# Performance work log

Hardware: AMD Instinct MI355X
Metric: run time of the kernel (lower is better)

Reference implementation:

```python
import jax, jax.numpy as jnp
import numpy as np

S, B, O, L, NL = 256, 64, 128, 256, 25
SIGMA_X, SIGMA_Z, ALPHA = 0.1, 0.1, 0.9


def setup_inputs() -> dict:
    key = jax.random.key(0)
    ks = jax.random.split(key, 12)
    def w(k, shape, s=0.05):
        return jax.random.normal(k, shape, dtype=jnp.float32) * s
    return {
        "obsrv": jax.random.normal(ks[0], (S, B, O), dtype=jnp.float32),
        "z0": jax.random.normal(ks[1], (NL, B, L), dtype=jnp.float32),
        "W_emb_z": w(ks[2], (L, L)), "b_emb_z": jnp.zeros((L,), jnp.float32),
        "Wx1": w(ks[3], (L, O)), "bx1": jnp.zeros((L,), jnp.float32),
        "Wx2": w(ks[4], (L, L)), "bx2": jnp.zeros((L,), jnp.float32),
        "Wx3": w(ks[5], (L, L)), "bx3": jnp.zeros((L,), jnp.float32),
        "W_ih": w(ks[6], (NL, 4 * L, L)), "W_hh": w(ks[7], (NL, 4 * L, L)),
        "b_ih": jnp.zeros((NL, 4 * L), jnp.float32),
        "b_hh": jnp.zeros((NL, 4 * L), jnp.float32),
        "W_out": w(ks[8], (L, L)), "b_out": jnp.zeros((L,), jnp.float32),
    }


def reference(obsrv, z0, W_emb_z, b_emb_z, Wx1, bx1, Wx2, bx2, Wx3, bx3,
              W_ih, W_hh, b_ih, b_hh, W_out, b_out):
    # Eval-mode LIDM forward: dropout disabled; noise injection kept (fixed PRNG).
    noise_key = jax.random.key(42)
    sqrt_alpha = jnp.sqrt(jnp.float32(ALPHA))

    def step(carry, inp):
        h, c = carry            # each [NL, B, L]
        x_k, k_idx = inp        # [B, O], scalar step index
        kh, kx = jax.random.split(jax.random.fold_in(noise_key, k_idx))
        # hidden = embedding_z(hidden) + sigma_z * noise
        h = jnp.einsum('nbl,ml->nbm', h, W_emb_z) + b_emb_z
        h = h + SIGMA_Z * jax.random.normal(kh, h.shape, dtype=h.dtype)
        # f_phi_x 3-layer MLP
        e = jax.nn.relu(x_k @ Wx1.T + bx1)
        e = jax.nn.relu(e @ Wx2.T + bx2)
        e = e @ Wx3.T + bx3
        e = sqrt_alpha * e + SIGMA_X * jax.random.normal(kx, e.shape, dtype=e.dtype)
        # 25-layer stacked LSTM, single time step (torch gate order i,f,g,o)
        inp_l = e
        hs, cs = [], []
        for l in range(NL):
            gates = inp_l @ W_ih[l].T + b_ih[l] + h[l] @ W_hh[l].T + b_hh[l]
            i, f, g, o = jnp.split(gates, 4, axis=-1)
            c_new = jax.nn.sigmoid(f) * c[l] + jax.nn.sigmoid(i) * jnp.tanh(g)
            h_new = jax.nn.sigmoid(o) * jnp.tanh(c_new)
            hs.append(h_new)
            cs.append(c_new)
            inp_l = h_new
        out = inp_l @ W_out.T + b_out
        return (jnp.stack(hs), jnp.stack(cs)), out

    c0 = jnp.zeros_like(z0)
    ks = jnp.arange(1, S)
    (_, _), ys = jax.lax.scan(step, (z0, c0), (obsrv[1:], ks))
    # outputs[0] stays zero, as in the torch module
    outputs = jnp.concatenate([jnp.zeros((1, B, L), ys.dtype), ys], axis=0)
    return outputs
```

## Files before the change

kernel.cpp:

```cpp
#include <hip/hip_runtime.h>
#include <stdint.h>

#define S_ 256
#define B_ 64
#define O_ 128
#define L_ 256
#define NL_ 25

typedef __attribute__((ext_vector_type(8))) short short8v;
typedef __attribute__((ext_vector_type(16))) float f32x16;
typedef __attribute__((ext_vector_type(4))) uint32_t u32x4;
typedef __attribute__((ext_vector_type(2))) uint32_t u32x2;

#define EMLP_B  0u
#define HL_B    8388608u
#define Z0P_B   16777216u
#define RING_B  17596416u
#define VBUF_B  24150016u
#define WF_B    37257216u
#define WN_B    50364416u
#define BIASF_B 63471616u
#define FLAG_B  63574016u
#define NFLAG_B 63580416u
#define WS_END  63626016u

#define GLDF(BV, BASE)                                                           \
  do {                                                                           \
    uint64_t a0_ = (uint64_t)(uintptr_t)(BASE);                                  \
    uint64_t a1_ = a0_ + 4096,  a2_ = a0_ + 8192,  a3_ = a0_ + 12288;            \
    uint64_t a4_ = a0_ + 16384, a5_ = a0_ + 20480, a6_ = a0_ + 24576;            \
    uint64_t a7_ = a0_ + 28672;                                                  \
    asm volatile("global_load_dwordx4 %0, %1, off sc0 sc1"             : "=v"(BV[0])  : "v"(a0_)); \
    asm volatile("global_load_dwordx4 %0, %1, off offset:2048 sc0 sc1" : "=v"(BV[1])  : "v"(a0_)); \
    asm volatile("global_load_dwordx4 %0, %1, off sc0 sc1"             : "=v"(BV[2])  : "v"(a1_)); \
    asm volatile("global_load_dwordx4 %0, %1, off offset:2048 sc0 sc1" : "=v"(BV[3])  : "v"(a1_)); \
    asm volatile("global_load_dwordx4 %0, %1, off sc0 sc1"             : "=v"(BV[4])  : "v"(a2_)); \
    asm volatile("global_load_dwordx4 %0, %1, off offset:2048 sc0 sc1" : "=v"(BV[5])  : "v"(a2_)); \
    asm volatile("global_load_dwordx4 %0, %1, off sc0 sc1"             : "=v"(BV[6])  : "v"(a3_)); \
    asm volatile("global_load_dwordx4 %0, %1, off offset:2048 sc0 sc1" : "=v"(BV[7])  : "v"(a3_)); \
    asm volatile("global_load_dwordx4 %0, %1, off sc0 sc1"             : "=v"(BV[8])  : "v"(a4_)); \
    asm volatile("global_load_dwordx4 %0, %1, off offset:2048 sc0 sc1" : "=v"(BV[9])  : "v"(a4_)); \
    asm volatile("global_load_dwordx4 %0, %1, off sc0 sc1"             : "=v"(BV[10]) : "v"(a5_)); \
    asm volatile("global_load_dwordx4 %0, %1, off offset:2048 sc0 sc1" : "=v"(BV[11]) : "v"(a5_)); \
    asm volatile("global_load_dwordx4 %0, %1, off sc0 sc1"             : "=v"(BV[12]) : "v"(a6_)); \
    asm volatile("global_load_dwordx4 %0, %1, off offset:2048 sc0 sc1" : "=v"(BV[13]) : "v"(a6_)); \
    asm volatile("global_load_dwordx4 %0, %1, off sc0 sc1"             : "=v"(BV[14]) : "v"(a7_)); \
    asm volatile("global_load_dwordx4 %0, %1, off offset:2048 sc0 sc1" : "=v"(BV[15]) : "v"(a7_)); \
  } while (0)

#define VMWAIT                                                                   \
  do {                                                                           \
    asm volatile("s_waitcnt vmcnt(0)" ::: "memory");                             \
    __builtin_amdgcn_sched_barrier(0);                                           \
  } while (0)

#define GST16(PTR, VAL)                                                          \
  do {                                                                           \
    uint64_t a_ = (uint64_t)(uintptr_t)(PTR);                                    \
    asm volatile("global_store_dwordx4 %0, %1, off sc0 sc1" :: "v"(a_), "v"(VAL) : "memory"); \
  } while (0)

#define GST8(PTR, VAL)                                                           \
  do {                                                                           \
    uint64_t a_ = (uint64_t)(uintptr_t)(PTR);                                    \
    asm volatile("global_store_dwordx2 %0, %1, off sc0 sc1" :: "v"(a_), "v"(VAL) : "memory"); \
  } while (0)

#define VMDRAIN asm volatile("s_waitcnt vmcnt(0)" ::: "memory")

__device__ __forceinline__ uint16_t f2bf(float x) {
  uint32_t u = __float_as_uint(x);
  return (uint16_t)((u + 0x7fffu + ((u >> 16) & 1u)) >> 16);
}
__device__ __forceinline__ float bf2f(uint16_t u) {
  return __uint_as_float(((uint32_t)u) << 16);
}
__device__ __forceinline__ short8v pack8(float4 a, float4 b) {
  short8v w;
  w[0] = (short)f2bf(a.x); w[1] = (short)f2bf(a.y);
  w[2] = (short)f2bf(a.z); w[3] = (short)f2bf(a.w);
  w[4] = (short)f2bf(b.x); w[5] = (short)f2bf(b.y);
  w[6] = (short)f2bf(b.z); w[7] = (short)f2bf(b.w);
  return w;
}

__device__ __forceinline__ uint32_t rotl32(uint32_t v, int r) {
  return (v << r) | (v >> (32 - r));
}

__device__ __forceinline__ void tf2x32(uint32_t k0, uint32_t k1,
                                       uint32_t x0, uint32_t x1,
                                       uint32_t& o0, uint32_t& o1) {
  uint32_t ks2 = k0 ^ k1 ^ 0x1BD11BDAu;
  x0 += k0; x1 += k1;
  x0 += x1; x1 = rotl32(x1, 13); x1 ^= x0;
  x0 += x1; x1 = rotl32(x1, 15); x1 ^= x0;
  x0 += x1; x1 = rotl32(x1, 26); x1 ^= x0;
  x0 += x1; x1 = rotl32(x1,  6); x1 ^= x0;
  x0 += k1; x1 += ks2 + 1u;
  x0 += x1; x1 = rotl32(x1, 17); x1 ^= x0;
  x0 += x1; x1 = rotl32(x1, 29); x1 ^= x0;
  x0 += x1; x1 = rotl32(x1, 16); x1 ^= x0;
  x0 += x1; x1 = rotl32(x1, 24); x1 ^= x0;
  x0 += ks2; x1 += k0 + 2u;
  x0 += x1; x1 = rotl32(x1, 13); x1 ^= x0;
  x0 += x1; x1 = rotl32(x1, 15); x1 ^= x0;
  x0 += x1; x1 = rotl32(x1, 26); x1 ^= x0;
  x0 += x1; x1 = rotl32(x1,  6); x1 ^= x0;
  x0 += k0; x1 += k1 + 3u;
  x0 += x1; x1 = rotl32(x1, 17); x1 ^= x0;
  x0 += x1; x1 = rotl32(x1, 29); x1 ^= x0;
  x0 += x1; x1 = rotl32(x1, 16); x1 ^= x0;
  x0 += x1; x1 = rotl32(x1, 24); x1 ^= x0;
  x0 += k1; x1 += ks2 + 4u;
  x0 += x1; x1 = rotl32(x1, 13); x1 ^= x0;
  x0 += x1; x1 = rotl32(x1, 15); x1 ^= x0;
  x0 += x1; x1 = rotl32(x1, 26); x1 ^= x0;
  x0 += x1; x1 = rotl32(x1,  6); x1 ^= x0;
  o0 = x0 + ks2; o1 = x1 + k0 + 5u;
}

__device__ __forceinline__ void step_keys(int k, uint32_t& kh0, uint32_t& kh1,
                                          uint32_t& kx0, uint32_t& kx1) {
  uint32_t f0, f1;
  tf2x32(0u, 42u, 0u, (uint32_t)k, f0, f1);
  tf2x32(f0, f1, 0u, 0u, kh0, kh1);
  tf2x32(f0, f1, 0u, 1u, kx0, kx1);
}

__device__ __forceinline__ uint32_t rbits(uint32_t key0, uint32_t key1,
                                          uint32_t i) {
  uint32_t b0, b1;
  tf2x32(key0, key1, 0u, i, b0, b1);
  return b0 ^ b1;
}

__device__ __forceinline__ float u32_to_normal(uint32_t bits) {
  const float lo = __uint_as_float(0xBF7FFFFFu);
  float f = __uint_as_float((bits >> 9) | 0x3F800000u) - 1.0f;
  float u = f * 2.0f + lo;
  u = fmaxf(lo, u);
  float x = u;
  float w = -log1pf(-x * x);
  float p;
  if (w < 5.0f) {
    w -= 2.5f;
    p =            2.81022636e-08f;
    p = fmaf(p, w, 3.43273939e-07f);
    p = fmaf(p, w, -3.5233877e-06f);
    p = fmaf(p, w, -4.39150654e-06f);
    p = fmaf(p, w, 0.00021858087f);
    p = fmaf(p, w, -0.00125372503f);
    p = fmaf(p, w, -0.00417768164f);
    p = fmaf(p, w, 0.246640727f);
    p = fmaf(p, w, 1.50140941f);
  } else {
    w = sqrtf(w) - 3.0f;
    p =            -0.000200214257f;
    p = fmaf(p, w, 0.000100950558f);
    p = fmaf(p, w, 0.00134934322f);
    p = fmaf(p, w, -0.00367342844f);
    p = fmaf(p, w, 0.00573950773f);
    p = fmaf(p, w, -0.0076224613f);
    p = fmaf(p, w, 0.00943887047f);
    p = fmaf(p, w, 1.00167406f);
    p = fmaf(p, w, 2.83297682f);
  }
  return __uint_as_float(0x3FB504F3u) * (p * x);
}

__device__ __forceinline__ float sigm(float x) { return 1.0f / (1.0f + expf(-x)); }

__device__ __forceinline__ uint64_t ld_u64_sc(const uint64_t* p) {
  uint64_t v;
  asm volatile("global_load_dwordx2 %0, %1, off sc0 sc1\n\ts_waitcnt vmcnt(0)"
               : "=v"(v) : "v"((uint64_t)(uintptr_t)p) : "memory");
  return v;
}
__device__ __forceinline__ uint32_t ld_u16_sc(const uint16_t* p) {
  uint32_t v;
  asm volatile("global_load_ushort %0, %1, off sc0 sc1\n\ts_waitcnt vmcnt(0)"
               : "=v"(v) : "v"((uint64_t)(uintptr_t)p) : "memory");
  return v;
}
__device__ __forceinline__ void spin_bytes_ge(const uint64_t* p, uint32_t want) {
  for (;;) {
    uint64_t v = ld_u64_sc(p);
    bool ok = true;
#pragma unroll
    for (int i = 0; i < 8; ++i) ok &= (uint32_t)((v >> (8 * i)) & 0xffu) >= want;
    if (ok) return;
    __builtin_amdgcn_s_sleep(4);
  }
}
__device__ __forceinline__ void spin_nf(const uint16_t* p, uint32_t pid) {
  uint32_t want = (pid & 0xffu) | ((pid & 0xffu) << 8);
  while (ld_u16_sc(p) != want) __builtin_amdgcn_s_sleep(4);
}
__device__ __forceinline__ void st_u8_sc(uint8_t* p, uint32_t v) {
  asm volatile("global_store_byte %0, %1, off sc0 sc1"
               :: "v"((uint64_t)(uintptr_t)p), "v"(v) : "memory");
}

__device__ __forceinline__ void gen_quarter(uint16_t* __restrict__ vbl,
                                            int l, int p, int s, int t, int q) {
  uint32_t kh0, kh1, kx0, kx1;
  step_keys(p, kh0, kh1, kx0, kx1);
  int vb = 32 * (s & 1) + (t >> 4);
  int fs = (t & 15) * 16 + q * 4;
  uint32_t ib = ((uint32_t)(l * 64 + vb)) * 256 + (uint32_t)fs;
  int g = fs >> 3;
  uint16_t* dst = vbl + (((size_t)(p & 15)) << 14) + ((size_t)(g * 64 + vb)) * 8 + (fs & 7);
  uint16_t n0 = f2bf(0.1f * u32_to_normal(rbits(kh0, kh1, ib + 0)));
  uint16_t n1 = f2bf(0.1f * u32_to_normal(rbits(kh0, kh1, ib + 1)));
  uint16_t n2 = f2bf(0.1f * u32_to_normal(rbits(kh0, kh1, ib + 2)));
  uint16_t n3 = f2bf(0.1f * u32_to_normal(rbits(kh0, kh1, ib + 3)));
  u32x2 dv;
  dv[0] = (uint32_t)n0 | ((uint32_t)n1 << 16);
  dv[1] = (uint32_t)n2 | ((uint32_t)n3 << 16);
  GST8(dst, dv);
}

__global__ __launch_bounds__(256) void k_init(const float* __restrict__ z0,
                                              uint16_t* __restrict__ z0p,
                                              uint32_t* __restrict__ fl) {
  int idx = blockIdx.x * 256 + threadIdx.x;
  int fi = idx & 255;
  int b = (idx >> 8) & 63;
  int l = idx >> 14;
  z0p[(((size_t)l * 32 + (fi >> 3)) * 64 + b) * 8 + (fi & 7)] = f2bf(z0[idx]);
  if (idx < 8000) fl[idx] = 0u;
}

__global__ __launch_bounds__(256) void k_wf(const float* __restrict__ Whh,
                                            const float* __restrict__ Wemb,
                                            uint16_t* __restrict__ Wf) {
  __shared__ float Bs[32][256];
  int l = blockIdx.x >> 4, rt = blockIdx.x & 15;
  int j = threadIdx.x;
  float acc[64];
#pragma unroll
  for (int r = 0; r < 64; ++r) acc[r] = 0.0f;
  const float* Abase = Whh + ((size_t)l * 1024 + rt * 64) * 256;
  for (int m0 = 0; m0 < 256; m0 += 32) {
    __syncthreads();
    {
      int rr = threadIdx.x >> 3, cseg = threadIdx.x & 7;
      const float* src = Wemb + (size_t)(m0 + rr) * 256 + cseg * 32;
      float* dst = &Bs[rr][cseg * 32];
#pragma unroll
      for (int q = 0; q < 8; ++q)
        reinterpret_cast<float4*>(dst)[q] = reinterpret_cast<const float4*>(src)[q];
    }
    __syncthreads();
    for (int mm = 0; mm < 32; ++mm) {
      float bj = Bs[mm][j];
      const float* Acol = Abase + m0 + mm;
#pragma unroll
      for (int r = 0; r < 64; ++r) acc[r] = fmaf(Acol[r * 256], bj, acc[r]);
    }
  }
  for (int r = 0; r < 64; ++r)
    Wf[((size_t)l * 1024 + rt * 64 + r) * 256 + j] = f2bf(acc[r]);
}

__global__ __launch_bounds__(256) void k_wn(const float* __restrict__ Whh,
                                            uint16_t* __restrict__ Wn) {
  int l = blockIdx.x >> 3, s = blockIdx.x & 7;
  uint16_t* base = Wn + ((size_t)(l * 8 + s) << 15);
  for (int it = 0; it < 16; ++it) {
    int c = it * 256 + threadIdx.x;
    int c2 = c >> 7;
    int r = c & 127;
    int gi = (r & 3) * 256 + s * 32 + (r >> 5) * 8 + ((r >> 2) & 7);
    const float* src = Whh + ((size_t)l * 1024 + gi) * 256 + c2 * 8;
    float4 f0 = *reinterpret_cast<const float4*>(src);
    float4 f1 = *reinterpret_cast<const float4*>(src + 4);
    *reinterpret_cast<short8v*>(base + (size_t)c * 8) = pack8(f0, f1);
  }
}

__global__ __launch_bounds__(256) void k_biasf(const float* __restrict__ Whh,
                                               const float* __restrict__ bemb,
                                               const float* __restrict__ bih,
                                               const float* __restrict__ bhh,
                                               float* __restrict__ biasf) {
  int l = blockIdx.x >> 2;
  int gi = (blockIdx.x & 3) * 256 + threadIdx.x;
  const float* row = Whh + ((size_t)l * 1024 + gi) * 256;
  float a = 0.0f;
  for (int m = 0; m < 256; ++m) a = fmaf(row[m], bemb[m], a);
  biasf[l * 1024 + gi] = a + bih[l * 1024 + gi] + bhh[l * 1024 + gi];
}

__global__ __launch_bounds__(256) void k_mlp1(const float* __restrict__ obsrv,
                                              const float* __restrict__ Wx1,
                                              const float* __restrict__ bx1,
                                              uint16_t* __restrict__ e1out) {
  int k = 1 + (blockIdx.x >> 2);
  int jc = blockIdx.x & 3;
  int lane = threadIdx.x & 63;
  int wv = threadIdx.x >> 6;
  int j0 = jc * 64 + wv * 16;
  const float* xrow = obsrv + ((size_t)k * B_ + lane) * O_;
  float acc[16];
#pragma unroll
  for (int i = 0; i < 16; ++i) acc[i] = 0.0f;
  for (int o = 0; o < O_; o += 4) {
    float4 a = *reinterpret_cast<const float4*>(&xrow[o]);
#pragma unroll
    for (int mi = 0; mi < 16; ++mi) {
      float4 wt = *reinterpret_cast<const float4*>(&Wx1[(size_t)(j0 + mi) * O_ + o]);
      float t = acc[mi];
      t = fmaf(a.x, wt.x, t); t = fmaf(a.y, wt.y, t);
      t = fmaf(a.z, wt.z, t); t = fmaf(a.w, wt.w, t);
      acc[mi] = t;
    }
  }
  uint16_t* dst = e1out + (size_t)k * L_ * B_;
#pragma unroll
  for (int mi = 0; mi < 16; ++mi) {
    float v = acc[mi] + bx1[j0 + mi];
    dst[(j0 + mi) * B_ + lane] = f2bf(fmaxf(v, 0.0f));
  }
}

__global__ __launch_bounds__(256) void k_mlp2(const uint16_t* __restrict__ e1buf,
                                              const float* __restrict__ Wx2,
                                              const float* __restrict__ bx2,
                                              const float* __restrict__ Wx3,
                                              const float* __restrict__ bx3,
                                              uint16_t* __restrict__ E_mlp) {
  __shared__ float e2s[L_ * B_];
  int k = 1 + blockIdx.x;
  int lane = threadIdx.x & 63;
  int wv = threadIdx.x >> 6;
  const uint16_t* e1 = e1buf + (size_t)k * L_ * B_;

  for (int rep = 0; rep < 4; ++rep) {
    int m0 = rep * 64 + wv * 16;
    float acc[16];
#pragma unroll
    for (int i = 0; i < 16; ++i) acc[i] = 0.0f;
    for (int j = 0; j < L_; j += 4) {
      float a0 = bf2f(e1[(j + 0) * B_ + lane]);
      float a1 = bf2f(e1[(j + 1) * B_ + lane]);
      float a2 = bf2f(e1[(j + 2) * B_ + lane]);
      float a3 = bf2f(e1[(j + 3) * B_ + lane]);
#pragma unroll
      for (int mi = 0; mi < 16; ++mi) {
        float4 wt = *reinterpret_cast<const float4*>(&Wx2[(size_t)(m0 + mi) * L_ + j]);
        float t = acc[mi];
        t = fmaf(a0, wt.x, t); t = fmaf(a1, wt.y, t);
        t = fmaf(a2, wt.z, t); t = fmaf(a3, wt.w, t);
        acc[mi] = t;
      }
    }
#pragma unroll
    for (int mi = 0; mi < 16; ++mi) {
      float v = acc[mi] + bx2[m0 + mi];
      e2s[(m0 + mi) * B_ + lane] = fmaxf(v, 0.0f);
    }
  }
  __syncthreads();

  uint32_t kh0, kh1, kx0, kx1;
  step_keys(k, kh0, kh1, kx0, kx1);
  const float sa = sqrtf(0.9f);

  for (int rep = 0; rep < 4; ++rep) {
    int m0 = rep * 64 + wv * 16;
    float acc[16];
#pragma unroll
    for (int i = 0; i < 16; ++i) acc[i] = 0.0f;
    for (int j = 0; j < L_; j += 4) {
      float a0 = e2s[(j + 0) * B_ + lane];
      float a1 = e2s[(j + 1) * B_ + lane];
      float a2 = e2s[(j + 2) * B_ + lane];
      float a3 = e2s[(j + 3) * B_ + lane];
#pragma unroll
      for (int mi = 0; mi < 16; ++mi) {
        float4 wt = *reinterpret_cast<const float4*>(&Wx3[(size_t)(m0 + mi) * L_ + j]);
        float t = acc[mi];
        t = fmaf(a0, wt.x, t); t = fmaf(a1, wt.y, t);
        t = fmaf(a2, wt.z, t); t = fmaf(a3, wt.w, t);
        acc[mi] = t;
      }
    }
    uint16_t tmp[16];
#pragma unroll
    for (int mi = 0; mi < 16; ++mi) {
      int m = m0 + mi;
      float nz = u32_to_normal(rbits(kx0, kx1, (uint32_t)(lane * L_ + m)));
      tmp[mi] = f2bf(sa * (acc[mi] + bx3[m]) + 0.1f * nz);
    }
    int g0 = m0 >> 3;
    uint16_t* d0 = E_mlp + (((size_t)k * 32 + g0) * 64 + lane) * 8;
    uint16_t* d1 = E_mlp + (((size_t)k * 32 + g0 + 1) * 64 + lane) * 8;
    *reinterpret_cast<uint4*>(d0) = *reinterpret_cast<const uint4*>(&tmp[0]);
    *reinterpret_cast<uint4*>(d1) = *reinterpret_cast<const uint4*>(&tmp[8]);
  }
}

__global__ __launch_bounds__(512, 1) void k_wave(
    const uint16_t* __restrict__ Wf, const float* __restrict__ W_ih,
    const uint16_t* __restrict__ Wn, const float* __restrict__ biasf,
    const uint16_t* __restrict__ z0p, const uint16_t* __restrict__ emlp,
    uint16_t* __restrict__ ring, uint16_t* __restrict__ vbuf,
    uint16_t* __restrict__ hlast, uint8_t* __restrict__ flagb,
    uint8_t* __restrict__ nfb) {
  __shared__ __align__(16) unsigned char WAF[65536];
  __shared__ __align__(16) unsigned char WAI[65536];

  const int slot = (blockIdx.x & 7) * 25 + (blockIdx.x >> 3);
  const int l = slot >> 3;
  const int s = slot & 7;
  const int t = threadIdx.x;
  const int lane = t & 63;
  const int wid = t >> 6;
  const int lo5 = lane & 31;
  const int hi = lane >> 5;
  const int tm = wid >> 1;
  const int tn = wid & 1;
  const int bcol = tn * 32 + lo5;
  const int arow = tm * 32 + lo5;
  const int aswz = (arow & 7) << 4;

#pragma unroll 1
  for (int it = 0; it < 8; ++it) {
    int c = it * 512 + t;
    int r = c >> 5, cc = c & 31;
    int gi = (r & 3) * 256 + s * 32 + (r >> 5) * 8 + ((r >> 2) & 7);
    uint4 v = *reinterpret_cast<const uint4*>(Wf + ((size_t)l * 1024 + gi) * 256 + cc * 8);
    *reinterpret_cast<uint4*>(WAF + r * 512 + ((cc * 16) ^ ((r & 7) << 4))) = v;
  }
#pragma unroll 1
  for (int it = 0; it < 8; ++it) {
    int c = it * 512 + t;
    int r = c >> 5, cc = c & 31;
    int gi = (r & 3) * 256 + s * 32 + (r >> 5) * 8 + ((r >> 2) & 7);
    const float* sr = W_ih + ((size_t)l * 1024 + gi) * 256 + cc * 8;
    float4 f0 = *reinterpret_cast<const float4*>(sr);
    float4 f1 = *reinterpret_cast<const float4*>(sr + 4);
    *reinterpret_cast<short8v*>(WAI + r * 512 + ((cc * 16) ^ ((r & 7) << 4))) = pack8(f0, f1);
  }

  float bfr[16];
#pragma unroll
  for (int mq = 0; mq < 4; ++mq) {
    int mi = s * 32 + tm * 8 + mq * 2 + hi;
#pragma unroll
    for (int g = 0; g < 4; ++g)
      bfr[mq * 4 + g] = biasf[l * 1024 + g * 256 + mi];
  }
  __syncthreads();

  uint16_t* vbl = vbuf + ((size_t)(l * 16) << 14);
  const uint16_t* wb = Wn + ((size_t)(l * 8 + s) << 15);
  const int blane = hi * 1024 + bcol * 16;
  const int ggrp = s * 4 + tm;

#define NFE(P) ((uint16_t*)(nfb + ((size_t)(l * 16 + ((P) & 15))) * 64))

#pragma unroll 1
  for (int g = 0; g < 2; ++g) {
    int p = 1 + g * 4 + (s >> 1);
#pragma unroll 1
    for (int q = 0; q < 4; ++q) gen_quarter(vbl, l, p, s, t, q);
    VMDRAIN;
    __syncthreads();
    if (t == 0) st_u8_sc((uint8_t*)NFE(p) + (s & 1), (uint32_t)(p & 0xff));
  }

  f32x16 nbt[4];
  float cst[4] = {0.0f, 0.0f, 0.0f, 0.0f};

#define PRO_NBT(ST, IDX)                                                         \
  do {                                                                           \
    if (t == 0) spin_nf(NFE(ST), (uint32_t)(ST));                                \
    __syncthreads();                                                             \
    const unsigned char* V = (const unsigned char*)vbl +                         \
        (((size_t)((ST) & 15)) << 15) + blane;                                   \
    short8v bv[16];                                                              \
    GLDF(bv, V);                                                                 \
    VMWAIT;                                                                      \
    f32x16 nw = {0,0,0,0,0,0,0,0,0,0,0,0,0,0,0,0};                               \
    _Pragma("unroll")                                                            \
    for (int kt = 0; kt < 16; ++kt) {                                            \
      short8v av = *reinterpret_cast<const short8v*>(                            \
          wb + ((size_t)((kt * 2 + hi) * 128 + arow)) * 8);                      \
      nw = __builtin_amdgcn_mfma_f32_32x32x16_bf16(av, bv[kt], nw, 0, 0, 0);     \
    }                                                                            \
    nbt[IDX] = nw;                                                               \
  } while (0)

  PRO_NBT(1, 0);
  PRO_NBT(2, 1);
  PRO_NBT(3, 2);
  PRO_NBT(4, 3);

#pragma unroll 1
  for (int k = 1; k <= 255; ++k) {
    if (t == 0 && k > 1) spin_bytes_ge((const uint64_t*)(flagb + l * 256), (uint32_t)(k - 1));
    if (t == 64 && l < NL_ - 1 && k >= 9)
      spin_bytes_ge((const uint64_t*)(flagb + (l + 1) * 256), (uint32_t)(k - 8));
    __syncthreads();

    const unsigned char* hp = (k == 1)
        ? ((const unsigned char*)z0p + (((size_t)l) << 15) + blane)
        : ((const unsigned char*)ring + (((size_t)(l * 8 + ((k - 1) & 7))) << 15) + blane);
    short8v bv0[16];
    GLDF(bv0, hp);

    if (t == 0 && l > 0) spin_bytes_ge((const uint64_t*)(flagb + (l - 1) * 256), (uint32_t)k);
    __syncthreads();
    VMWAIT;

    const unsigned char* ip = (l == 0)
        ? ((const unsigned char*)emlp + (((size_t)k) << 15) + blane)
        : ((const unsigned char*)ring + (((size_t)((l - 1) * 8 + (k & 7))) << 15) + blane);
    short8v bv1[16];
    GLDF(bv1, ip);

    f32x16 acc = nbt[0];
#pragma unroll
    for (int kt = 0; kt < 16; ++kt) {
      short8v av = *reinterpret_cast<const short8v*>(WAF + arow * 512 + ((kt * 32 + hi * 16) ^ aswz));
      acc = __builtin_amdgcn_mfma_f32_32x32x16_bf16(av, bv0[kt], acc, 0, 0, 0);
    }
    VMWAIT;
#pragma unroll
    for (int kt = 0; kt < 16; ++kt) {
      short8v av = *reinterpret_cast<const short8v*>(WAI + arow * 512 + ((kt * 32 + hi * 16) ^ aswz));
      acc = __builtin_amdgcn_mfma_f32_32x32x16_bf16(av, bv1[kt], acc, 0, 0, 0);
    }

    uint16_t hv[4];
#pragma unroll
    for (int mq = 0; mq < 4; ++mq) {
      float iv = acc[4 * mq + 0] + bfr[mq * 4 + 0];
      float fv = acc[4 * mq + 1] + bfr[mq * 4 + 1];
      float gv = acc[4 * mq + 2] + bfr[mq * 4 + 2];
      float ov = acc[4 * mq + 3] + bfr[mq * 4 + 3];
      float cn = sigm(fv) * cst[mq] + sigm(iv) * tanhf(gv);
      float hn = sigm(ov) * tanhf(cn);
      cst[mq] = cn;
      hv[mq] = f2bf(hn);
      if (l == NL_ - 1) {
        int mi = s * 32 + tm * 8 + mq * 2 + hi;
        hlast[((size_t)k << 14) + mi * 64 + bcol] = hv[mq];
      }
    }
    {
      uint32_t w0 = (uint32_t)hv[0] | ((uint32_t)hv[1] << 16);
      uint32_t w1 = (uint32_t)hv[2] | ((uint32_t)hv[3] << 16);
      uint32_t p0 = (uint32_t)__shfl_xor((int)w0, 32);
      uint32_t p1 = (uint32_t)__shfl_xor((int)w1, 32);
      if (hi == 0) {
        u32x4 dv;
        dv[0] = (w0 & 0xffffu) | (p0 << 16);
        dv[1] = (w0 >> 16) | (p0 & 0xffff0000u);
        dv[2] = (w1 & 0xffffu) | (p1 << 16);
        dv[3] = (w1 >> 16) | (p1 & 0xffff0000u);
        unsigned char* rp = (unsigned char*)ring +
            (((size_t)(l * 8 + (k & 7))) << 15) + ((size_t)(ggrp * 64 + bcol)) * 16;
        GST16(rp, dv);
      }
    }
    VMDRAIN;
    __syncthreads();
    if (t == 0) st_u8_sc(flagb + l * 256 + s, (uint32_t)(k & 0xff));

    {
      int base = ((k - 1) & ~3) + 1;
      int q = (k - 1) & 3;
      int p = base + 8 + (s >> 1);
      if (p <= 255) {
        gen_quarter(vbl, l, p, s, t, q);
        if (q == 3) {
          VMDRAIN;
          __syncthreads();
          if (t == 0) st_u8_sc((uint8_t*)NFE(p) + (s & 1), (uint32_t)(p & 0xff));
        }
      }
    }
    {
      int kn = k + 4;
      f32x16 nw = {0,0,0,0,0,0,0,0,0,0,0,0,0,0,0,0};
      if (kn <= 255) {
        if (t == 0) spin_nf(NFE(kn), (uint32_t)kn);
        __syncthreads();
        const unsigned char* V = (const unsigned char*)vbl +
            (((size_t)(kn & 15)) << 15) + blane;
        short8v bv[16];
        GLDF(bv, V);
        VMWAIT;
#pragma unroll
        for (int kt = 0; kt < 16; ++kt) {
          short8v av = *reinterpret_cast<const short8v*>(
              wb + ((size_t)((kt * 2 + hi) * 128 + arow)) * 8);
          nw = __builtin_amdgcn_mfma_f32_32x32x16_bf16(av, bv[kt], nw, 0, 0, 0);
        }
      }
      nbt[0] = nbt[1]; nbt[1] = nbt[2]; nbt[2] = nbt[3]; nbt[3] = nw;
    }
  }
#undef NFE
#undef PRO_NBT
}

__global__ __launch_bounds__(256) void k_final(const uint16_t* __restrict__ Hlast,
                                               const float* __restrict__ W_out,
                                               const float* __restrict__ b_out,
                                               float* __restrict__ out) {
  int k = blockIdx.x >> 2;
  int mc = blockIdx.x & 3;
  int lane = threadIdx.x & 63;
  int wv = threadIdx.x >> 6;
  int m0 = mc * 64 + wv * 16;
  float res[16];
  if (k == 0) {
#pragma unroll
    for (int mi = 0; mi < 16; ++mi) res[mi] = 0.0f;
  } else {
    float acc[16];
#pragma unroll
    for (int i = 0; i < 16; ++i) acc[i] = 0.0f;
    const uint16_t* src = Hlast + ((size_t)k << 14);
    for (int j = 0; j < L_; j += 4) {
      float a0 = bf2f(src[(j + 0) * B_ + lane]);
      float a1 = bf2f(src[(j + 1) * B_ + lane]);
      float a2 = bf2f(src[(j + 2) * B_ + lane]);
      float a3 = bf2f(src[(j + 3) * B_ + lane]);
#pragma unroll
      for (int mi = 0; mi < 16; ++mi) {
        float4 wt = *reinterpret_cast<const float4*>(&W_out[(size_t)(m0 + mi) * L_ + j]);
        float t = acc[mi];
        t = fmaf(a0, wt.x, t); t = fmaf(a1, wt.y, t);
        t = fmaf(a2, wt.z, t); t = fmaf(a3, wt.w, t);
        acc[mi] = t;
      }
    }
#pragma unroll
    for (int mi = 0; mi < 16; ++mi) res[mi] = acc[mi] + b_out[m0 + mi];
  }
  float* dst = out + ((size_t)k * B_ + lane) * L_ + m0;
#pragma unroll
  for (int v = 0; v < 4; ++v) {
    float4 t4 = make_float4(res[4 * v], res[4 * v + 1], res[4 * v + 2], res[4 * v + 3]);
    *reinterpret_cast<float4*>(&dst[4 * v]) = t4;
  }
}

extern "C" void kernel_launch(void* const* d_in, const int* in_sizes, int n_in,
                              void* d_out, int out_size, void* d_ws, size_t ws_size,
                              hipStream_t stream) {
  const float* obsrv = (const float*)d_in[0];
  const float* z0    = (const float*)d_in[1];
  const float* W_emb = (const float*)d_in[2];
  const float* b_emb = (const float*)d_in[3];
  const float* Wx1   = (const float*)d_in[4];
  const float* bx1   = (const float*)d_in[5];
  const float* Wx2   = (const float*)d_in[6];
  const float* bx2   = (const float*)d_in[7];
  const float* Wx3   = (const float*)d_in[8];
  const float* bx3   = (const float*)d_in[9];
  const float* W_ih  = (const float*)d_in[10];
  const float* W_hh  = (const float*)d_in[11];
  const float* b_ih  = (const float*)d_in[12];
  const float* b_hh  = (const float*)d_in[13];
  const float* W_out = (const float*)d_in[14];
  const float* b_out = (const float*)d_in[15];
  float* out = (float*)d_out;
  unsigned char* ws = (unsigned char*)d_ws;

  if (ws_size < (size_t)WS_END) return;

  uint16_t* E_mlp = (uint16_t*)(ws + EMLP_B);
  uint16_t* e1tmp = (uint16_t*)(ws + HL_B);
  uint16_t* Hlast = (uint16_t*)(ws + HL_B);
  uint16_t* z0p   = (uint16_t*)(ws + Z0P_B);
  uint16_t* ring  = (uint16_t*)(ws + RING_B);
  uint16_t* vbuf  = (uint16_t*)(ws + VBUF_B);
  uint16_t* Wf    = (uint16_t*)(ws + WF_B);
  uint16_t* Wn    = (uint16_t*)(ws + WN_B);
  float*    biasf = (float*)(ws + BIASF_B);
  uint8_t*  flagb = (uint8_t*)(ws + FLAG_B);
  uint8_t*  nfb   = (uint8_t*)(ws + NFLAG_B);

  k_init<<<1600, 256, 0, stream>>>(z0, z0p, (uint32_t*)(ws + FLAG_B));
  k_wf<<<25 * 16, 256, 0, stream>>>(W_hh, W_emb, Wf);
  k_wn<<<25 * 8, 256, 0, stream>>>(W_hh, Wn);
  k_biasf<<<25 * 4, 256, 0, stream>>>(W_hh, b_emb, b_ih, b_hh, biasf);
  k_mlp1<<<255 * 4, 256, 0, stream>>>(obsrv, Wx1, bx1, e1tmp);
  k_mlp2<<<255, 256, 0, stream>>>(e1tmp, Wx2, bx2, Wx3, bx3, E_mlp);

  void* args[] = {(void*)&Wf, (void*)&W_ih, (void*)&Wn, (void*)&biasf,
                  (void*)&z0p, (void*)&E_mlp, (void*)&ring, (void*)&vbuf,
                  (void*)&Hlast, (void*)&flagb, (void*)&nfb};
  hipLaunchCooperativeKernel((const void*)k_wave, dim3(NL_ * 8), dim3(512),
                             args, 0, stream);

  k_final<<<S_ * 4, 256, 0, stream>>>(Hlast, W_out, b_out, out);
}
```

Measured before the change: 4.217 ms.

## Stage shared B panels through LDS instead of per-wave redundant global loads

Previously every wave loaded its own B-operand fragments for the h, input and noise panels straight from global memory with cache-bypassing loads, so waves sharing the same columns fetched the same data several times. Now the whole 512-thread block loads each 32KB panel once (four dwordx4 per thread) into a new LDS staging buffer, and each wave then reads its MFMA fragments from LDS. This removes the duplicated coherent global traffic on the serial recurrence path. The cost is extra block-wide barriers and an LDS round trip on every step, and the LDS footprint grows to 160KB.

```diff
diff --git a/kernel.cpp b/kernel.cpp
--- a/kernel.cpp
+++ b/kernel.cpp
@@ -24,30 +24,6 @@
 #define NFLAG_B 63580416u
 #define WS_END  63626016u
 
-#define GLDF(BV, BASE)                                                           \
-  do {                                                                           \
-    uint64_t a0_ = (uint64_t)(uintptr_t)(BASE);                                  \
-    uint64_t a1_ = a0_ + 4096,  a2_ = a0_ + 8192,  a3_ = a0_ + 12288;            \
-    uint64_t a4_ = a0_ + 16384, a5_ = a0_ + 20480, a6_ = a0_ + 24576;            \
-    uint64_t a7_ = a0_ + 28672;                                                  \
-    asm volatile("global_load_dwordx4 %0, %1, off sc0 sc1"             : "=v"(BV[0])  : "v"(a0_)); \
-    asm volatile("global_load_dwordx4 %0, %1, off offset:2048 sc0 sc1" : "=v"(BV[1])  : "v"(a0_)); \
-    asm volatile("global_load_dwordx4 %0, %1, off sc0 sc1"             : "=v"(BV[2])  : "v"(a1_)); \
-    asm volatile("global_load_dwordx4 %0, %1, off offset:2048 sc0 sc1" : "=v"(BV[3])  : "v"(a1_)); \
-    asm volatile("global_load_dwordx4 %0, %1, off sc0 sc1"             : "=v"(BV[4])  : "v"(a2_)); \
-    asm volatile("global_load_dwordx4 %0, %1, off offset:2048 sc0 sc1" : "=v"(BV[5])  : "v"(a2_)); \
-    asm volatile("global_load_dwordx4 %0, %1, off sc0 sc1"             : "=v"(BV[6])  : "v"(a3_)); \
-    asm volatile("global_load_dwordx4 %0, %1, off offset:2048 sc0 sc1" : "=v"(BV[7])  : "v"(a3_)); \
-    asm volatile("global_load_dwordx4 %0, %1, off sc0 sc1"             : "=v"(BV[8])  : "v"(a4_)); \
-    asm volatile("global_load_dwordx4 %0, %1, off offset:2048 sc0 sc1" : "=v"(BV[9])  : "v"(a4_)); \
-    asm volatile("global_load_dwordx4 %0, %1, off sc0 sc1"             : "=v"(BV[10]) : "v"(a5_)); \
-    asm volatile("global_load_dwordx4 %0, %1, off offset:2048 sc0 sc1" : "=v"(BV[11]) : "v"(a5_)); \
-    asm volatile("global_load_dwordx4 %0, %1, off sc0 sc1"             : "=v"(BV[12]) : "v"(a6_)); \
-    asm volatile("global_load_dwordx4 %0, %1, off offset:2048 sc0 sc1" : "=v"(BV[13]) : "v"(a6_)); \
-    asm volatile("global_load_dwordx4 %0, %1, off sc0 sc1"             : "=v"(BV[14]) : "v"(a7_)); \
-    asm volatile("global_load_dwordx4 %0, %1, off offset:2048 sc0 sc1" : "=v"(BV[15]) : "v"(a7_)); \
-  } while (0)
-
 #define VMWAIT                                                                   \
   do {                                                                           \
     asm volatile("s_waitcnt vmcnt(0)" ::: "memory");                             \
@@ -67,6 +43,42 @@
   } while (0)
 
 #define VMDRAIN asm volatile("s_waitcnt vmcnt(0)" ::: "memory")
+
+#define PANEL_LD(R0, R1, R2, R3, BASE)                                           \
+  do {                                                                           \
+    uint64_t a0_ = (uint64_t)(uintptr_t)(BASE) + (uint32_t)(t * 16);             \
+    uint64_t a1_ = a0_ + 8192, a2_ = a0_ + 16384, a3_ = a0_ + 24576;             \
+    asm volatile("global_load_dwordx4 %0, %1, off sc0 sc1" : "=v"(R0) : "v"(a0_)); \
+    asm volatile("global_load_dwordx4 %0, %1, off sc0 sc1" : "=v"(R1) : "v"(a1_)); \
+    asm volatile("global_load_dwordx4 %0, %1, off sc0 sc1" : "=v"(R2) : "v"(a2_)); \
+    asm volatile("global_load_dwordx4 %0, %1, off sc0 sc1" : "=v"(R3) : "v"(a3_)); \
+  } while (0)
+
+#define PANEL_ST(R0, R1, R2, R3)                                                 \
+  do {                                                                           \
+    *reinterpret_cast<u32x4*>(ST + t * 16)         = R0;                         \
+    *reinterpret_cast<u32x4*>(ST + 8192 + t * 16)  = R1;                         \
+    *reinterpret_cast<u32x4*>(ST + 16384 + t * 16) = R2;                         \
+    *reinterpret_cast<u32x4*>(ST + 24576 + t * 16) = R3;                         \
+  } while (0)
+
+#define PANEL_RD(BV)                                                             \
+  do {                                                                           \
+    _Pragma("unroll")                                                            \
+    for (int kt_ = 0; kt_ < 16; ++kt_)                                           \
+      BV[kt_] = *reinterpret_cast<const short8v*>(ST + kt_ * 2048 + blane);      \
+  } while (0)
+
+#define STAGE_PANEL(BV, GBASE)                                                   \
+  do {                                                                           \
+    u32x4 r0_, r1_, r2_, r3_;                                                    \
+    PANEL_LD(r0_, r1_, r2_, r3_, GBASE);                                         \
+    VMWAIT;                                                                      \
+    __syncthreads();                                                             \
+    PANEL_ST(r0_, r1_, r2_, r3_);                                                \
+    __syncthreads();                                                             \
+    PANEL_RD(BV);                                                                \
+  } while (0)
 
 __device__ __forceinline__ uint16_t f2bf(float x) {
   uint32_t u = __float_as_uint(x);
@@ -409,8 +421,10 @@
     uint16_t* __restrict__ ring, uint16_t* __restrict__ vbuf,
     uint16_t* __restrict__ hlast, uint8_t* __restrict__ flagb,
     uint8_t* __restrict__ nfb) {
-  __shared__ __align__(16) unsigned char WAF[65536];
-  __shared__ __align__(16) unsigned char WAI[65536];
+  __shared__ __align__(16) unsigned char SMEM[163840];
+  unsigned char* WAF = SMEM;
+  unsigned char* WAI = SMEM + 65536;
+  unsigned char* ST  = SMEM + 131072;
 
   const int slot = (blockIdx.x & 7) * 25 + (blockIdx.x >> 3);
   const int l = slot >> 3;
@@ -475,29 +489,23 @@
   f32x16 nbt[4];
   float cst[4] = {0.0f, 0.0f, 0.0f, 0.0f};
 
-#define PRO_NBT(ST, IDX)                                                         \
-  do {                                                                           \
-    if (t == 0) spin_nf(NFE(ST), (uint32_t)(ST));                                \
-    __syncthreads();                                                             \
-    const unsigned char* V = (const unsigned char*)vbl +                         \
-        (((size_t)((ST) & 15)) << 15) + blane;                                   \
-    short8v bv[16];                                                              \
-    GLDF(bv, V);                                                                 \
-    VMWAIT;                                                                      \
-    f32x16 nw = {0,0,0,0,0,0,0,0,0,0,0,0,0,0,0,0};                               \
-    _Pragma("unroll")                                                            \
-    for (int kt = 0; kt < 16; ++kt) {                                            \
-      short8v av = *reinterpret_cast<const short8v*>(                            \
-          wb + ((size_t)((kt * 2 + hi) * 128 + arow)) * 8);                      \
-      nw = __builtin_amdgcn_mfma_f32_32x32x16_bf16(av, bv[kt], nw, 0, 0, 0);     \
-    }                                                                            \
-    nbt[IDX] = nw;                                                               \
-  } while (0)
-
-  PRO_NBT(1, 0);
-  PRO_NBT(2, 1);
-  PRO_NBT(3, 2);
-  PRO_NBT(4, 3);
+#pragma unroll 1
+  for (int st = 1; st <= 4; ++st) {
+    if (t == 0) spin_nf(NFE(st), (uint32_t)st);
+    short8v bv[16];
+    STAGE_PANEL(bv, (const unsigned char*)vbl + (((size_t)(st & 15)) << 15));
+    f32x16 nw = {0,0,0,0,0,0,0,0,0,0,0,0,0,0,0,0};
+#pragma unroll
+    for (int kt = 0; kt < 16; ++kt) {
+      short8v av = *reinterpret_cast<const short8v*>(
+          wb + ((size_t)((kt * 2 + hi) * 128 + arow)) * 8);
+      nw = __builtin_amdgcn_mfma_f32_32x32x16_bf16(av, bv[kt], nw, 0, 0, 0);
+    }
+    if (st == 1) nbt[0] = nw;
+    else if (st == 2) nbt[1] = nw;
+    else if (st == 3) nbt[2] = nw;
+    else nbt[3] = nw;
+  }
 
 #pragma unroll 1
   for (int k = 1; k <= 255; ++k) {
@@ -507,20 +515,25 @@
     __syncthreads();
 
     const unsigned char* hp = (k == 1)
-        ? ((const unsigned char*)z0p + (((size_t)l) << 15) + blane)
-        : ((const unsigned char*)ring + (((size_t)(l * 8 + ((k - 1) & 7))) << 15) + blane);
+        ? ((const unsigned char*)z0p + (((size_t)l) << 15))
+        : ((const unsigned char*)ring + (((size_t)(l * 8 + ((k - 1) & 7))) << 15));
+    u32x4 h0, h1, h2, h3;
+    PANEL_LD(h0, h1, h2, h3, hp);
+
+    if (t == 0 && l > 0) spin_bytes_ge((const uint64_t*)(flagb + (l - 1) * 256), (uint32_t)k);
+    VMWAIT;
+    __syncthreads();
+    PANEL_ST(h0, h1, h2, h3);
+    __syncthreads();
+
     short8v bv0[16];
-    GLDF(bv0, hp);
-
-    if (t == 0 && l > 0) spin_bytes_ge((const uint64_t*)(flagb + (l - 1) * 256), (uint32_t)k);
-    __syncthreads();
-    VMWAIT;
+    PANEL_RD(bv0);
 
     const unsigned char* ip = (l == 0)
-        ? ((const unsigned char*)emlp + (((size_t)k) << 15) + blane)
-        : ((const unsigned char*)ring + (((size_t)((l - 1) * 8 + (k & 7))) << 15) + blane);
-    short8v bv1[16];
-    GLDF(bv1, ip);
+        ? ((const unsigned char*)emlp + (((size_t)k) << 15))
+        : ((const unsigned char*)ring + (((size_t)((l - 1) * 8 + (k & 7))) << 15));
+    u32x4 i0, i1, i2, i3;
+    PANEL_LD(i0, i1, i2, i3, ip);
 
     f32x16 acc = nbt[0];
 #pragma unroll
@@ -529,6 +542,12 @@
       acc = __builtin_amdgcn_mfma_f32_32x32x16_bf16(av, bv0[kt], acc, 0, 0, 0);
     }
     VMWAIT;
+    __syncthreads();
+    PANEL_ST(i0, i1, i2, i3);
+    __syncthreads();
+
+    short8v bv1[16];
+    PANEL_RD(bv1);
 #pragma unroll
     for (int kt = 0; kt < 16; ++kt) {
       short8v av = *reinterpret_cast<const short8v*>(WAI + arow * 512 + ((kt * 32 + hi * 16) ^ aswz));
@@ -589,12 +608,8 @@
       f32x16 nw = {0,0,0,0,0,0,0,0,0,0,0,0,0,0,0,0};
       if (kn <= 255) {
         if (t == 0) spin_nf(NFE(kn), (uint32_t)kn);
-        __syncthreads();
-        const unsigned char* V = (const unsigned char*)vbl +
-            (((size_t)(kn & 15)) << 15) + blane;
         short8v bv[16];
-        GLDF(bv, V);
-        VMWAIT;
+        STAGE_PANEL(bv, (const unsigned char*)vbl + (((size_t)(kn & 15)) << 15));
 #pragma unroll
         for (int kt = 0; kt < 16; ++kt) {
           short8v av = *reinterpret_cast<const short8v*>(
@@ -606,7 +621,6 @@
     }
   }
 #undef NFE
-#undef PRO_NBT
 }
 
 __global__ __launch_bounds__(256) void k_final(const uint16_t* __restrict__ Hlast,
```

New measurement: 5.384 ms. 1.28x slower.
